# Performance work log

Measured on AMD Instinct MI355X. Metric: run time of the kernel, lower is better.

The kernel has to match this reference:

```python
import jax, jax.numpy as jnp
import numpy as np

N = 50000      # nodes
E = 800000     # edges
F_IN = 128     # num_node_features
H = 128        # dim_h
C = 5          # num_classes
G = 8          # graphs in batch


def setup_inputs() -> dict:
    key = jax.random.key(0)
    ks = jax.random.split(key, 9)
    x = jax.random.normal(ks[0], (N, F_IN), dtype=jnp.float32)
    edge_index = jax.random.randint(ks[1], (2, E), 0, N, dtype=jnp.int64)
    batch = jnp.sort(jax.random.randint(ks[2], (N,), 0, G, dtype=jnp.int64))
    s1 = 1.0 / np.sqrt(F_IN)
    s2 = 1.0 / np.sqrt(H)
    sl = 1.0 / np.sqrt(2 * H)
    W1 = jax.random.uniform(ks[3], (F_IN, H), jnp.float32, -s1, s1)
    b1 = jnp.zeros((H,), jnp.float32)
    W2 = jax.random.uniform(ks[4], (H, H), jnp.float32, -s2, s2)
    b2 = jnp.zeros((H,), jnp.float32)
    Wl = jax.random.uniform(ks[5], (2 * H, C), jnp.float32, -sl, sl)
    bl = jax.random.uniform(ks[6], (C,), jnp.float32, -sl, sl)
    return {"x": x, "edge_index": edge_index, "batch": batch,
            "W1": W1, "b1": b1, "W2": W2, "b2": b2, "Wl": Wl, "bl": bl}


def gcn_conv(x, W, b, src, dst):
    # PyG GCNConv: X' = D^{-1/2} (A + I) D^{-1/2} X W + b
    xw = x @ W                                           # [N, H]
    # degree with self-loops: 1 + in-degree
    deg = jnp.ones((N,), xw.dtype).at[dst].add(1.0)      # [N]
    dinv = jax.lax.rsqrt(deg)                            # [N]
    norm = dinv[src] * dinv[dst]                         # [E]
    msg = xw[src] * norm[:, None]                        # [E, H] gather
    agg = jax.ops.segment_sum(msg, dst, num_segments=N)  # scatter-add
    agg = agg + xw * (dinv * dinv)[:, None]              # self-loop term
    return agg + b


def reference(x, edge_index, batch, W1, b1, W2, b2, Wl, bl):
    src, dst = edge_index[0], edge_index[1]
    # dropout p=0.6 is a no-op in eval mode
    h1 = jax.nn.relu(gcn_conv(x, W1, b1, src, dst))
    h2 = jax.nn.relu(gcn_conv(h1, W2, b2, src, dst))
    h = jnp.concatenate([h2, h1], axis=-1)               # [N, 2H]
    cnt = jax.ops.segment_sum(jnp.ones((N,), h.dtype), batch, num_segments=G)
    hG = jax.ops.segment_sum(h, batch, num_segments=G) / jnp.maximum(cnt, 1.0)[:, None]
    logits = hG @ Wl + bl                                # [G, C]
    return hG, jax.nn.log_softmax(logits, axis=1)
```

## Files before the change

### kernel.cpp

```cpp
#include <hip/hip_runtime.h>

#define N_NODES 50000
#define N_EDGES 800000
#define HDIM    128
#define NGRAPH  8
#define NCLS    5
#define SCAN_CHUNK 1024
#define NSCANBLK ((N_NODES + SCAN_CHUNK - 1) / SCAN_CHUNK)
#define NB_GEMM  ((N_NODES + 63) / 64)
#define NB_EDGE  ((N_EDGES + 255) / 256)

__device__ __forceinline__ float bf2f(ushort u) {
    return __uint_as_float((unsigned int)u << 16);
}
__device__ __forceinline__ ushort f2bf(float f) {
    unsigned int u = __float_as_uint(f);
    u += 0x7FFFu + ((u >> 16) & 1u);
    return (ushort)(u >> 16);
}

typedef __attribute__((ext_vector_type(8)))  __bf16 bf16x8;
typedef __attribute__((ext_vector_type(16))) float  f32x16;
union BF8 { uint4 q; ushort u[8]; bf16x8 v; };

__global__ __launch_bounds__(256) void k_pre(const float* __restrict__ x,
                                             ushort* __restrict__ xb,
                                             const float* __restrict__ W1,
                                             const float* __restrict__ W2,
                                             ushort* __restrict__ Wt1,
                                             ushort* __restrict__ Wt2,
                                             int* cnti, float* hG) {
    int i = blockIdx.x * blockDim.x + threadIdx.x;
    if (i < N_NODES) cnti[i] = 0;
    if (i < NGRAPH * 2 * HDIM) hG[i] = 0.0f;
    if (i < HDIM * HDIM) {
        int k = i >> 7, c = i & (HDIM - 1);
        Wt1[c * HDIM + k] = f2bf(W1[i]);
        Wt2[c * HDIM + k] = f2bf(W2[i]);
    }
    if ((size_t)i * 8 < (size_t)N_NODES * HDIM) {
        float4 f0 = reinterpret_cast<const float4*>(x)[i * 2];
        float4 f1 = reinterpret_cast<const float4*>(x)[i * 2 + 1];
        uint4 o;
        o.x = (unsigned)f2bf(f0.x) | ((unsigned)f2bf(f0.y) << 16);
        o.y = (unsigned)f2bf(f0.z) | ((unsigned)f2bf(f0.w) << 16);
        o.z = (unsigned)f2bf(f1.x) | ((unsigned)f2bf(f1.y) << 16);
        o.w = (unsigned)f2bf(f1.z) | ((unsigned)f2bf(f1.w) << 16);
        reinterpret_cast<uint4*>(xb)[i] = o;
    }
}

__global__ __launch_bounds__(256) void k_count(const int* __restrict__ dst,
                                               int* cnti,
                                               ushort* __restrict__ slot16) {
    int e = blockIdx.x * blockDim.x + threadIdx.x;
    if (e < N_EDGES)
        slot16[e] = (ushort)atomicAdd(&cnti[dst[e]], 1);
}

__global__ __launch_bounds__(256) void k_scan1(const int* __restrict__ cnti,
                                               int* __restrict__ rowptr,
                                               int* __restrict__ bsum,
                                               float* __restrict__ dinv) {
    __shared__ int wsum[4];
    int tid = threadIdx.x, lane = tid & 63, wid = tid >> 6;
    int i0 = blockIdx.x * SCAN_CHUNK + tid * 4;
    int v[4];
    int tsum = 0;
#pragma unroll
    for (int p = 0; p < 4; ++p) {
        int i = i0 + p;
        v[p] = (i < N_NODES) ? cnti[i] : 0;
        if (i < N_NODES) dinv[i] = rsqrtf(1.0f + (float)v[p]);
        tsum += v[p];
    }
    int sc = tsum;
#pragma unroll
    for (int off = 1; off < 64; off <<= 1) {
        int t = __shfl_up(sc, off, 64);
        if (lane >= off) sc += t;
    }
    if (lane == 63) wsum[wid] = sc;
    __syncthreads();
    int woff = 0;
    for (int w = 0; w < wid; ++w) woff += wsum[w];
    int excl = woff + sc - tsum;
#pragma unroll
    for (int p = 0; p < 4; ++p) {
        int i = i0 + p;
        if (i < N_NODES) rowptr[i] = excl;
        excl += v[p];
    }
    if (tid == 255) bsum[blockIdx.x] = woff + sc;
}

__global__ __launch_bounds__(64) void k_scan2(int* __restrict__ bsum,
                                              int* __restrict__ rowptr) {
    int t = threadIdx.x;
    int v = (t < NSCANBLK) ? bsum[t] : 0;
    int sc = v;
#pragma unroll
    for (int off = 1; off < 64; off <<= 1) {
        int x = __shfl_up(sc, off, 64);
        if (t >= off) sc += x;
    }
    if (t < NSCANBLK) bsum[t] = sc - v;
    if (t == NSCANBLK - 1) rowptr[N_NODES] = sc;
}

__global__ __launch_bounds__(256) void k_scan3(int* __restrict__ rowptr,
                                               const int* __restrict__ bsum) {
    int i = blockIdx.x * blockDim.x + threadIdx.x;
    if (i < N_NODES) rowptr[i] += bsum[i >> 10];
}

__global__ __launch_bounds__(256) void k_gemm_fill(const ushort* __restrict__ Xb,
                                                   const ushort* __restrict__ Wt,
                                                   ushort* __restrict__ Y,
                                                   const int* __restrict__ src,
                                                   const int* __restrict__ dst,
                                                   const int* __restrict__ rowptr,
                                                   const ushort* __restrict__ slot16,
                                                   ushort* __restrict__ csrc16) {
    if (blockIdx.x >= NB_GEMM) {
        int e = (blockIdx.x - NB_GEMM) * 256 + threadIdx.x;
        if (e < N_EDGES) {
            int d = dst[e];
            int pos = rowptr[d] + (int)slot16[e];
            csrc16[pos] = (ushort)src[e];
        }
        return;
    }
    int tid  = threadIdx.x;
    int lane = tid & 63;
    int wv   = tid >> 6;
    int c0   = wv * 32;
    int lrow = lane & 31;
    int kgrp = lane >> 5;

    bf16x8 bfrag[8];
    {
        const ushort* wp = Wt + (size_t)(c0 + lrow) * HDIM + kgrp * 8;
#pragma unroll
        for (int kc = 0; kc < 8; ++kc) {
            BF8 t;
            t.q = *reinterpret_cast<const uint4*>(wp + kc * 16);
            bfrag[kc] = t.v;
        }
    }
#pragma unroll
    for (int chunk = 0; chunk < 2; ++chunk) {
        int m0 = blockIdx.x * 64 + chunk * 32;
        if (m0 >= N_NODES) return;
        int arow = m0 + lrow;
        if (arow > N_NODES - 1) arow = N_NODES - 1;
        const ushort* xp = Xb + (size_t)arow * HDIM + kgrp * 8;
        f32x16 acc;
#pragma unroll
        for (int i = 0; i < 16; ++i) acc[i] = 0.f;
#pragma unroll
        for (int kc = 0; kc < 8; ++kc) {
            BF8 a;
            a.q = *reinterpret_cast<const uint4*>(xp + kc * 16);
            acc = __builtin_amdgcn_mfma_f32_32x32x16_bf16(a.v, bfrag[kc], acc, 0, 0, 0);
        }
#pragma unroll
        for (int r = 0; r < 16; ++r) {
            int row = m0 + (r & 3) + 8 * (r >> 2) + 4 * kgrp;
            if (row < N_NODES)
                Y[(size_t)row * HDIM + c0 + lrow] = f2bf(acc[r]);
        }
    }
}

__global__ __launch_bounds__(256) void k_gemm(const ushort* __restrict__ Xb,
                                              const ushort* __restrict__ Wt,
                                              ushort* __restrict__ Y) {
    int tid  = threadIdx.x;
    int lane = tid & 63;
    int wv   = tid >> 6;
    int c0   = wv * 32;
    int lrow = lane & 31;
    int kgrp = lane >> 5;

    bf16x8 bfrag[8];
    {
        const ushort* wp = Wt + (size_t)(c0 + lrow) * HDIM + kgrp * 8;
#pragma unroll
        for (int kc = 0; kc < 8; ++kc) {
            BF8 t;
            t.q = *reinterpret_cast<const uint4*>(wp + kc * 16);
            bfrag[kc] = t.v;
        }
    }
#pragma unroll
    for (int chunk = 0; chunk < 2; ++chunk) {
        int m0 = blockIdx.x * 64 + chunk * 32;
        if (m0 >= N_NODES) return;
        int arow = m0 + lrow;
        if (arow > N_NODES - 1) arow = N_NODES - 1;
        const ushort* xp = Xb + (size_t)arow * HDIM + kgrp * 8;
        f32x16 acc;
#pragma unroll
        for (int i = 0; i < 16; ++i) acc[i] = 0.f;
#pragma unroll
        for (int kc = 0; kc < 8; ++kc) {
            BF8 a;
            a.q = *reinterpret_cast<const uint4*>(xp + kc * 16);
            acc = __builtin_amdgcn_mfma_f32_32x32x16_bf16(a.v, bfrag[kc], acc, 0, 0, 0);
        }
#pragma unroll
        for (int r = 0; r < 16; ++r) {
            int row = m0 + (r & 3) + 8 * (r >> 2) + 4 * kgrp;
            if (row < N_NODES)
                Y[(size_t)row * HDIM + c0 + lrow] = f2bf(acc[r]);
        }
    }
}

__global__ __launch_bounds__(256) void k_agg(const ushort* __restrict__ y,
                                             const int* __restrict__ rowptr,
                                             const ushort* __restrict__ csrc16,
                                             const float* __restrict__ dinv,
                                             const float* __restrict__ bias,
                                             ushort* __restrict__ h) {
    int node = blockIdx.x * 4 + (threadIdx.x >> 6);
    if (node >= N_NODES) return;
    int lane = threadIdx.x & 63;
    int e0 = rowptr[node], e1 = rowptr[node + 1];
    float a0 = 0.f, a1 = 0.f, b0 = 0.f, b1 = 0.f;
    float c0 = 0.f, c1 = 0.f, d0 = 0.f, d1 = 0.f;
    int j = e0;
    for (; j + 8 <= e1; j += 8) {
        int s0 = csrc16[j],     s1 = csrc16[j + 1], s2 = csrc16[j + 2], s3 = csrc16[j + 3];
        int s4 = csrc16[j + 4], s5 = csrc16[j + 5], s6 = csrc16[j + 6], s7 = csrc16[j + 7];
        float w0 = dinv[s0], w1 = dinv[s1], w2 = dinv[s2], w3 = dinv[s3];
        float w4 = dinv[s4], w5 = dinv[s5], w6 = dinv[s6], w7 = dinv[s7];
        ushort2 v0 = *reinterpret_cast<const ushort2*>(y + (size_t)s0 * HDIM + lane * 2);
        ushort2 v1 = *reinterpret_cast<const ushort2*>(y + (size_t)s1 * HDIM + lane * 2);
        ushort2 v2 = *reinterpret_cast<const ushort2*>(y + (size_t)s2 * HDIM + lane * 2);
        ushort2 v3 = *reinterpret_cast<const ushort2*>(y + (size_t)s3 * HDIM + lane * 2);
        ushort2 v4 = *reinterpret_cast<const ushort2*>(y + (size_t)s4 * HDIM + lane * 2);
        ushort2 v5 = *reinterpret_cast<const ushort2*>(y + (size_t)s5 * HDIM + lane * 2);
        ushort2 v6 = *reinterpret_cast<const ushort2*>(y + (size_t)s6 * HDIM + lane * 2);
        ushort2 v7 = *reinterpret_cast<const ushort2*>(y + (size_t)s7 * HDIM + lane * 2);
        a0 = fmaf(w0, bf2f(v0.x), a0); a1 = fmaf(w0, bf2f(v0.y), a1);
        b0 = fmaf(w1, bf2f(v1.x), b0); b1 = fmaf(w1, bf2f(v1.y), b1);
        c0 = fmaf(w2, bf2f(v2.x), c0); c1 = fmaf(w2, bf2f(v2.y), c1);
        d0 = fmaf(w3, bf2f(v3.x), d0); d1 = fmaf(w3, bf2f(v3.y), d1);
        a0 = fmaf(w4, bf2f(v4.x), a0); a1 = fmaf(w4, bf2f(v4.y), a1);
        b0 = fmaf(w5, bf2f(v5.x), b0); b1 = fmaf(w5, bf2f(v5.y), b1);
        c0 = fmaf(w6, bf2f(v6.x), c0); c1 = fmaf(w6, bf2f(v6.y), c1);
        d0 = fmaf(w7, bf2f(v7.x), d0); d1 = fmaf(w7, bf2f(v7.y), d1);
    }
    for (; j + 4 <= e1; j += 4) {
        int s0 = csrc16[j], s1 = csrc16[j + 1], s2 = csrc16[j + 2], s3 = csrc16[j + 3];
        float w0 = dinv[s0], w1 = dinv[s1], w2 = dinv[s2], w3 = dinv[s3];
        ushort2 v0 = *reinterpret_cast<const ushort2*>(y + (size_t)s0 * HDIM + lane * 2);
        ushort2 v1 = *reinterpret_cast<const ushort2*>(y + (size_t)s1 * HDIM + lane * 2);
        ushort2 v2 = *reinterpret_cast<const ushort2*>(y + (size_t)s2 * HDIM + lane * 2);
        ushort2 v3 = *reinterpret_cast<const ushort2*>(y + (size_t)s3 * HDIM + lane * 2);
        a0 = fmaf(w0, bf2f(v0.x), a0); a1 = fmaf(w0, bf2f(v0.y), a1);
        b0 = fmaf(w1, bf2f(v1.x), b0); b1 = fmaf(w1, bf2f(v1.y), b1);
        c0 = fmaf(w2, bf2f(v2.x), c0); c1 = fmaf(w2, bf2f(v2.y), c1);
        d0 = fmaf(w3, bf2f(v3.x), d0); d1 = fmaf(w3, bf2f(v3.y), d1);
    }
    for (; j < e1; ++j) {
        int s = csrc16[j];
        float w = dinv[s];
        ushort2 v = *reinterpret_cast<const ushort2*>(y + (size_t)s * HDIM + lane * 2);
        a0 = fmaf(w, bf2f(v.x), a0); a1 = fmaf(w, bf2f(v.y), a1);
    }
    float di = dinv[node];
    ushort2 vs = *reinterpret_cast<const ushort2*>(y + (size_t)node * HDIM + lane * 2);
    a0 = fmaf(di, bf2f(vs.x), a0); a1 = fmaf(di, bf2f(vs.y), a1);
    float s0 = (a0 + b0) + (c0 + d0);
    float s1 = (a1 + b1) + (c1 + d1);
    float r0 = fmaxf(fmaf(s0, di, bias[lane * 2]),     0.f);
    float r1 = fmaxf(fmaf(s1, di, bias[lane * 2 + 1]), 0.f);
    ushort2 res; res.x = f2bf(r0); res.y = f2bf(r1);
    *reinterpret_cast<ushort2*>(h + (size_t)node * HDIM + lane * 2) = res;
}

__global__ __launch_bounds__(256) void k_pool(const ushort* __restrict__ h2,
                                              const ushort* __restrict__ h1,
                                              const int* __restrict__ batch,
                                              float* __restrict__ hG) {
    int f  = threadIdx.x;
    const ushort* srcp = (f < HDIM) ? h2 : h1;
    int ff = f & (HDIM - 1);
    int n0 = blockIdx.x * 64;
    int n1 = min(n0 + 64, N_NODES);
    int g = batch[n0];
    float run = 0.f;
    for (int n = n0; n < n1; ++n) {
        int gn = batch[n];
        if (gn != g) {
            atomicAdd(&hG[g * 256 + f], run);
            run = 0.f;
            g = gn;
        }
        run += bf2f(srcp[(size_t)n * HDIM + ff]);
    }
    atomicAdd(&hG[g * 256 + f], run);
}

__global__ __launch_bounds__(256) void k_final(const float* __restrict__ hG,
                                               const int* __restrict__ batch,
                                               const float* __restrict__ Wl,
                                               const float* __restrict__ bl,
                                               float* __restrict__ outp) {
    __shared__ float sH[NGRAPH * 2 * HDIM];
    __shared__ float sL[NGRAPH * NCLS];
    __shared__ int   sStart[NGRAPH + 1];
    int tid = threadIdx.x;
    if (tid <= NGRAPH) {
        int lo = 0, hi = N_NODES;
        while (lo < hi) {
            int mid = (lo + hi) >> 1;
            if (batch[mid] < tid) lo = mid + 1; else hi = mid;
        }
        sStart[tid] = lo;
    }
    __syncthreads();
    for (int i = tid; i < NGRAPH * 2 * HDIM; i += 256) {
        int g = i >> 8;
        float cnt = (float)(sStart[g + 1] - sStart[g]);
        float m = hG[i] / fmaxf(cnt, 1.0f);
        sH[i] = m;
        outp[i] = m;
    }
    __syncthreads();
    if (tid < NGRAPH * NCLS) {
        int g = tid / NCLS, c = tid % NCLS;
        float acc = bl[c];
        for (int k = 0; k < 2 * HDIM; ++k)
            acc += sH[g * 256 + k] * Wl[k * NCLS + c];
        sL[tid] = acc;
    }
    __syncthreads();
    if (tid < NGRAPH) {
        float mx = -1e30f;
        for (int c = 0; c < NCLS; ++c) mx = fmaxf(mx, sL[tid * NCLS + c]);
        float se = 0.f;
        for (int c = 0; c < NCLS; ++c) se += expf(sL[tid * NCLS + c] - mx);
        float lse = logf(se) + mx;
        for (int c = 0; c < NCLS; ++c)
            outp[NGRAPH * 2 * HDIM + tid * NCLS + c] = sL[tid * NCLS + c] - lse;
    }
}

extern "C" void kernel_launch(void* const* d_in, const int* in_sizes, int n_in,
                              void* d_out, int out_size, void* d_ws, size_t ws_size,
                              hipStream_t stream) {
    const float* x    = (const float*)d_in[0];
    const int*   eidx = (const int*)d_in[1];
    const int*   batch= (const int*)d_in[2];
    const float* W1   = (const float*)d_in[3];
    const float* b1   = (const float*)d_in[4];
    const float* W2   = (const float*)d_in[5];
    const float* b2   = (const float*)d_in[6];
    const float* Wl   = (const float*)d_in[7];
    const float* bl   = (const float*)d_in[8];
    float* outp = (float*)d_out;

    const int* src = eidx;
    const int* dst = eidx + N_EDGES;

    char* ws = (char*)d_ws;
    size_t off = 0;
    auto alloc = [&](size_t bytes) -> char* {
        char* p = ws + off;
        off += (bytes + 255) & ~(size_t)255;
        return p;
    };
    ushort* xb    = (ushort*)alloc((size_t)N_NODES * HDIM * 2);
    ushort* y     = (ushort*)alloc((size_t)N_NODES * HDIM * 2);
    ushort* h1    = (ushort*)alloc((size_t)N_NODES * HDIM * 2);
    ushort* h2    = (ushort*)alloc((size_t)N_NODES * HDIM * 2);
    ushort* Wt1   = (ushort*)alloc((size_t)HDIM * HDIM * 2);
    ushort* Wt2   = (ushort*)alloc((size_t)HDIM * HDIM * 2);
    float*  dinv  = (float*) alloc((size_t)N_NODES * 4);
    int*    cnti  = (int*)   alloc((size_t)N_NODES * 4);
    int*    rowptr= (int*)   alloc((size_t)(N_NODES + 1) * 4);
    int*    bsum  = (int*)   alloc((size_t)NSCANBLK * 4);
    ushort* slot16= (ushort*)alloc((size_t)N_EDGES * 2);
    ushort* csrc16= (ushort*)alloc((size_t)N_EDGES * 2);
    float*  hG    = (float*) alloc((size_t)NGRAPH * 2 * HDIM * 4);

    k_pre  <<<(N_NODES * HDIM / 8 + 255) / 256, 256, 0, stream>>>(x, xb, W1, W2, Wt1, Wt2, cnti, hG);
    k_count<<<NB_EDGE, 256, 0, stream>>>(dst, cnti, slot16);
    k_scan1<<<NSCANBLK, 256, 0, stream>>>(cnti, rowptr, bsum, dinv);
    k_scan2<<<1, 64, 0, stream>>>(bsum, rowptr);
    k_scan3<<<(N_NODES + 255) / 256, 256, 0, stream>>>(rowptr, bsum);

    k_gemm_fill<<<NB_GEMM + NB_EDGE, 256, 0, stream>>>(xb, Wt1, y,
                                                       src, dst, rowptr, slot16, csrc16);
    k_agg <<<(N_NODES + 3) / 4, 256, 0, stream>>>(y, rowptr, csrc16, dinv, b1, h1);
    k_gemm<<<NB_GEMM, 256, 0, stream>>>(h1, Wt2, y);
    k_agg <<<(N_NODES + 3) / 4, 256, 0, stream>>>(y, rowptr, csrc16, dinv, b2, h2);

    k_pool <<<(N_NODES + 63) / 64, 256, 0, stream>>>(h2, h1, batch, hG);
    k_final<<<1, 256, 0, stream>>>(hG, batch, Wl, bl, outp);

    (void)in_sizes; (void)n_in; (void)out_size; (void)ws_size;
}
```

Before: 200.6 us.

## Split GEMM output into column quarters and restructure aggregation per quarter

Result: slower. 294.8 us (median of 2 runs) (+46.9%).

```diff
diff --git a/kernel.cpp b/kernel.cpp
--- a/kernel.cpp
+++ b/kernel.cpp
@@ -9,6 +9,7 @@
 #define NSCANBLK ((N_NODES + SCAN_CHUNK - 1) / SCAN_CHUNK)
 #define NB_GEMM  ((N_NODES + 63) / 64)
 #define NB_EDGE  ((N_EDGES + 255) / 256)
+#define QSTRIDE  ((size_t)N_NODES * 32)
 
 __device__ __forceinline__ float bf2f(ushort u) {
     return __uint_as_float((unsigned int)u << 16);
@@ -53,9 +54,16 @@
 __global__ __launch_bounds__(256) void k_count(const int* __restrict__ dst,
                                                int* cnti,
                                                ushort* __restrict__ slot16) {
-    int e = blockIdx.x * blockDim.x + threadIdx.x;
-    if (e < N_EDGES)
-        slot16[e] = (ushort)atomicAdd(&cnti[dst[e]], 1);
+    int e4 = blockIdx.x * blockDim.x + threadIdx.x;
+    if (e4 < N_EDGES / 4) {
+        int4 d = reinterpret_cast<const int4*>(dst)[e4];
+        ushort4 s;
+        s.x = (ushort)atomicAdd(&cnti[d.x], 1);
+        s.y = (ushort)atomicAdd(&cnti[d.y], 1);
+        s.z = (ushort)atomicAdd(&cnti[d.z], 1);
+        s.w = (ushort)atomicAdd(&cnti[d.w], 1);
+        reinterpret_cast<ushort4*>(slot16)[e4] = s;
+    }
 }
 
 __global__ __launch_bounds__(256) void k_scan1(const int* __restrict__ cnti,
@@ -94,24 +102,21 @@
     if (tid == 255) bsum[blockIdx.x] = woff + sc;
 }
 
-__global__ __launch_bounds__(64) void k_scan2(int* __restrict__ bsum,
-                                              int* __restrict__ rowptr) {
-    int t = threadIdx.x;
-    int v = (t < NSCANBLK) ? bsum[t] : 0;
-    int sc = v;
-#pragma unroll
-    for (int off = 1; off < 64; off <<= 1) {
-        int x = __shfl_up(sc, off, 64);
-        if (t >= off) sc += x;
-    }
-    if (t < NSCANBLK) bsum[t] = sc - v;
-    if (t == NSCANBLK - 1) rowptr[N_NODES] = sc;
-}
-
 __global__ __launch_bounds__(256) void k_scan3(int* __restrict__ rowptr,
                                                const int* __restrict__ bsum) {
-    int i = blockIdx.x * blockDim.x + threadIdx.x;
-    if (i < N_NODES) rowptr[i] += bsum[i >> 10];
+    __shared__ int soff;
+    int tid = threadIdx.x;
+    int chunk = blockIdx.x >> 2;
+    if (tid < 64) {
+        int v = (tid < chunk) ? bsum[tid] : 0;
+#pragma unroll
+        for (int off = 32; off; off >>= 1) v += __shfl_xor(v, off, 64);
+        if (tid == 0) soff = v;
+    }
+    __syncthreads();
+    int i = blockIdx.x * 256 + tid;
+    if (i < N_NODES) rowptr[i] += soff;
+    if (blockIdx.x == 0 && tid == 0) rowptr[N_NODES] = N_EDGES;
 }
 
 __global__ __launch_bounds__(256) void k_gemm_fill(const ushort* __restrict__ Xb,
@@ -134,13 +139,12 @@
     int tid  = threadIdx.x;
     int lane = tid & 63;
     int wv   = tid >> 6;
-    int c0   = wv * 32;
     int lrow = lane & 31;
     int kgrp = lane >> 5;
 
     bf16x8 bfrag[8];
     {
-        const ushort* wp = Wt + (size_t)(c0 + lrow) * HDIM + kgrp * 8;
+        const ushort* wp = Wt + (size_t)(wv * 32 + lrow) * HDIM + kgrp * 8;
 #pragma unroll
         for (int kc = 0; kc < 8; ++kc) {
             BF8 t;
@@ -168,7 +172,8 @@
         for (int r = 0; r < 16; ++r) {
             int row = m0 + (r & 3) + 8 * (r >> 2) + 4 * kgrp;
             if (row < N_NODES)
-                Y[(size_t)row * HDIM + c0 + lrow] = f2bf(acc[r]);
+                __builtin_nontemporal_store(f2bf(acc[r]),
+                    Y + (size_t)wv * QSTRIDE + (size_t)row * 32 + lrow);
         }
     }
 }
@@ -179,13 +184,12 @@
     int tid  = threadIdx.x;
     int lane = tid & 63;
     int wv   = tid >> 6;
-    int c0   = wv * 32;
     int lrow = lane & 31;
     int kgrp = lane >> 5;
 
     bf16x8 bfrag[8];
     {
-        const ushort* wp = Wt + (size_t)(c0 + lrow) * HDIM + kgrp * 8;
+        const ushort* wp = Wt + (size_t)(wv * 32 + lrow) * HDIM + kgrp * 8;
 #pragma unroll
         for (int kc = 0; kc < 8; ++kc) {
             BF8 t;
@@ -213,7 +217,8 @@
         for (int r = 0; r < 16; ++r) {
             int row = m0 + (r & 3) + 8 * (r >> 2) + 4 * kgrp;
             if (row < N_NODES)
-                Y[(size_t)row * HDIM + c0 + lrow] = f2bf(acc[r]);
+                __builtin_nontemporal_store(f2bf(acc[r]),
+                    Y + (size_t)wv * QSTRIDE + (size_t)row * 32 + lrow);
         }
     }
 }
@@ -227,59 +232,47 @@
     int node = blockIdx.x * 4 + (threadIdx.x >> 6);
     if (node >= N_NODES) return;
     int lane = threadIdx.x & 63;
+    int grp  = lane >> 4;
+    int fl   = lane & 15;
     int e0 = rowptr[node], e1 = rowptr[node + 1];
-    float a0 = 0.f, a1 = 0.f, b0 = 0.f, b1 = 0.f;
-    float c0 = 0.f, c1 = 0.f, d0 = 0.f, d1 = 0.f;
-    int j = e0;
-    for (; j + 8 <= e1; j += 8) {
-        int s0 = csrc16[j],     s1 = csrc16[j + 1], s2 = csrc16[j + 2], s3 = csrc16[j + 3];
-        int s4 = csrc16[j + 4], s5 = csrc16[j + 5], s6 = csrc16[j + 6], s7 = csrc16[j + 7];
-        float w0 = dinv[s0], w1 = dinv[s1], w2 = dinv[s2], w3 = dinv[s3];
-        float w4 = dinv[s4], w5 = dinv[s5], w6 = dinv[s6], w7 = dinv[s7];
-        ushort2 v0 = *reinterpret_cast<const ushort2*>(y + (size_t)s0 * HDIM + lane * 2);
-        ushort2 v1 = *reinterpret_cast<const ushort2*>(y + (size_t)s1 * HDIM + lane * 2);
-        ushort2 v2 = *reinterpret_cast<const ushort2*>(y + (size_t)s2 * HDIM + lane * 2);
-        ushort2 v3 = *reinterpret_cast<const ushort2*>(y + (size_t)s3 * HDIM + lane * 2);
-        ushort2 v4 = *reinterpret_cast<const ushort2*>(y + (size_t)s4 * HDIM + lane * 2);
-        ushort2 v5 = *reinterpret_cast<const ushort2*>(y + (size_t)s5 * HDIM + lane * 2);
-        ushort2 v6 = *reinterpret_cast<const ushort2*>(y + (size_t)s6 * HDIM + lane * 2);
-        ushort2 v7 = *reinterpret_cast<const ushort2*>(y + (size_t)s7 * HDIM + lane * 2);
-        a0 = fmaf(w0, bf2f(v0.x), a0); a1 = fmaf(w0, bf2f(v0.y), a1);
-        b0 = fmaf(w1, bf2f(v1.x), b0); b1 = fmaf(w1, bf2f(v1.y), b1);
-        c0 = fmaf(w2, bf2f(v2.x), c0); c1 = fmaf(w2, bf2f(v2.y), c1);
-        d0 = fmaf(w3, bf2f(v3.x), d0); d1 = fmaf(w3, bf2f(v3.y), d1);
-        a0 = fmaf(w4, bf2f(v4.x), a0); a1 = fmaf(w4, bf2f(v4.y), a1);
-        b0 = fmaf(w5, bf2f(v5.x), b0); b1 = fmaf(w5, bf2f(v5.y), b1);
-        c0 = fmaf(w6, bf2f(v6.x), c0); c1 = fmaf(w6, bf2f(v6.y), c1);
-        d0 = fmaf(w7, bf2f(v7.x), d0); d1 = fmaf(w7, bf2f(v7.y), d1);
-    }
-    for (; j + 4 <= e1; j += 4) {
-        int s0 = csrc16[j], s1 = csrc16[j + 1], s2 = csrc16[j + 2], s3 = csrc16[j + 3];
-        float w0 = dinv[s0], w1 = dinv[s1], w2 = dinv[s2], w3 = dinv[s3];
-        ushort2 v0 = *reinterpret_cast<const ushort2*>(y + (size_t)s0 * HDIM + lane * 2);
-        ushort2 v1 = *reinterpret_cast<const ushort2*>(y + (size_t)s1 * HDIM + lane * 2);
-        ushort2 v2 = *reinterpret_cast<const ushort2*>(y + (size_t)s2 * HDIM + lane * 2);
-        ushort2 v3 = *reinterpret_cast<const ushort2*>(y + (size_t)s3 * HDIM + lane * 2);
-        a0 = fmaf(w0, bf2f(v0.x), a0); a1 = fmaf(w0, bf2f(v0.y), a1);
-        b0 = fmaf(w1, bf2f(v1.x), b0); b1 = fmaf(w1, bf2f(v1.y), b1);
-        c0 = fmaf(w2, bf2f(v2.x), c0); c1 = fmaf(w2, bf2f(v2.y), c1);
-        d0 = fmaf(w3, bf2f(v3.x), d0); d1 = fmaf(w3, bf2f(v3.y), d1);
-    }
-    for (; j < e1; ++j) {
-        int s = csrc16[j];
-        float w = dinv[s];
-        ushort2 v = *reinterpret_cast<const ushort2*>(y + (size_t)s * HDIM + lane * 2);
-        a0 = fmaf(w, bf2f(v.x), a0); a1 = fmaf(w, bf2f(v.y), a1);
-    }
     float di = dinv[node];
-    ushort2 vs = *reinterpret_cast<const ushort2*>(y + (size_t)node * HDIM + lane * 2);
-    a0 = fmaf(di, bf2f(vs.x), a0); a1 = fmaf(di, bf2f(vs.y), a1);
-    float s0 = (a0 + b0) + (c0 + d0);
-    float s1 = (a1 + b1) + (c1 + d1);
-    float r0 = fmaxf(fmaf(s0, di, bias[lane * 2]),     0.f);
-    float r1 = fmaxf(fmaf(s1, di, bias[lane * 2 + 1]), 0.f);
-    ushort2 res; res.x = f2bf(r0); res.y = f2bf(r1);
-    *reinterpret_cast<ushort2*>(h + (size_t)node * HDIM + lane * 2) = res;
+#pragma unroll
+    for (int q = 0; q < 4; ++q) {
+        const ushort* yq = y + (size_t)q * QSTRIDE;
+        float a0 = 0.f, a1 = 0.f;
+        int j = e0;
+        for (; j + 16 <= e1; j += 16) {
+#pragma unroll
+            for (int u = 0; u < 4; ++u) {
+                int s = (int)csrc16[j + u * 4 + grp];
+                float w = dinv[s];
+                ushort2 v = *reinterpret_cast<const ushort2*>(yq + (size_t)s * 32 + fl * 2);
+                a0 = fmaf(w, bf2f(v.x), a0);
+                a1 = fmaf(w, bf2f(v.y), a1);
+            }
+        }
+        for (; j < e1; j += 4) {
+            int jj = j + grp;
+            bool valid = jj < e1;
+            int s = valid ? (int)csrc16[jj] : 0;
+            float w = valid ? dinv[s] : 0.f;
+            ushort2 v = *reinterpret_cast<const ushort2*>(yq + (size_t)s * 32 + fl * 2);
+            a0 = fmaf(w, bf2f(v.x), a0);
+            a1 = fmaf(w, bf2f(v.y), a1);
+        }
+        a0 += __shfl_xor(a0, 16, 64); a1 += __shfl_xor(a1, 16, 64);
+        a0 += __shfl_xor(a0, 32, 64); a1 += __shfl_xor(a1, 32, 64);
+        ushort2 vs = *reinterpret_cast<const ushort2*>(yq + (size_t)node * 32 + fl * 2);
+        a0 = fmaf(di, bf2f(vs.x), a0);
+        a1 = fmaf(di, bf2f(vs.y), a1);
+        float r0 = fmaxf(fmaf(a0, di, bias[q * 32 + fl * 2]),     0.f);
+        float r1 = fmaxf(fmaf(a1, di, bias[q * 32 + fl * 2 + 1]), 0.f);
+        if (grp == 0) {
+            unsigned pk = (unsigned)f2bf(r0) | ((unsigned)f2bf(r1) << 16);
+            __builtin_nontemporal_store(pk,
+                reinterpret_cast<unsigned*>(h + (size_t)node * HDIM + q * 32 + fl * 2));
+        }
+    }
 }
 
 __global__ __launch_bounds__(256) void k_pool(const ushort* __restrict__ h2,
@@ -389,9 +382,8 @@
     float*  hG    = (float*) alloc((size_t)NGRAPH * 2 * HDIM * 4);
 
     k_pre  <<<(N_NODES * HDIM / 8 + 255) / 256, 256, 0, stream>>>(x, xb, W1, W2, Wt1, Wt2, cnti, hG);
-    k_count<<<NB_EDGE, 256, 0, stream>>>(dst, cnti, slot16);
+    k_count<<<(N_EDGES / 4 + 255) / 256, 256, 0, stream>>>(dst, cnti, slot16);
     k_scan1<<<NSCANBLK, 256, 0, stream>>>(cnti, rowptr, bsum, dinv);
-    k_scan2<<<1, 64, 0, stream>>>(bsum, rowptr);
     k_scan3<<<(N_NODES + 255) / 256, 256, 0, stream>>>(rowptr, bsum);
 
     k_gemm_fill<<<NB_GEMM + NB_EDGE, 256, 0, stream>>>(xb, Wt1, y,
```
